# Kernel tuning notes

Measured on AMD Instinct MI355X. Metric: run time of the kernel, lower is better.

## Reference

```python
import jax, jax.numpy as jnp
import numpy as np


def setup_inputs() -> dict:
    key = jax.random.key(0)
    ks = jax.random.split(key, 7)
    T, B, D, H, F = 1024, 128, 256, 256, 128
    inputs = jax.random.normal(ks[0], (T, B, D), dtype=jnp.float32)
    # stacked gate linears (forget, input, update, output): [D+H, 4H]
    Wg = jax.random.normal(ks[1], (D + H, 4 * H), dtype=jnp.float32) / np.sqrt(D + H)
    bg = jax.random.normal(ks[2], (4 * H,), dtype=jnp.float32) * 0.01
    # stacked per-gate FFNs: Linear(H->F), ReLU, Linear(F->H), sigmoid/tanh
    W1 = jax.random.normal(ks[3], (4, H, F), dtype=jnp.float32) / np.sqrt(H)
    b1 = jax.random.normal(ks[4], (4, F), dtype=jnp.float32) * 0.01
    W2 = jax.random.normal(ks[5], (4, F, H), dtype=jnp.float32) / np.sqrt(F)
    b2 = jax.random.normal(ks[6], (4, H), dtype=jnp.float32) * 0.01
    return {"inputs": inputs, "Wg": Wg, "bg": bg, "W1": W1, "b1": b1, "W2": W2, "b2": b2}


def reference(inputs, Wg, bg, W1, b1, W2, b2):
    T, B, D = inputs.shape
    H = W2.shape[-1]

    def step(carry, x):
        hx, cx = carry
        comb = jnp.concatenate([x, hx], axis=1)              # [B, D+H]
        z = (comb @ Wg + bg).reshape(B, 4, H)                # stacked gate linears
        z = jnp.transpose(z, (1, 0, 2))                      # [4, B, H]
        h1 = jax.nn.relu(jnp.einsum('gbh,ghf->gbf', z, W1) + b1[:, None, :])
        z2 = jnp.einsum('gbf,gfh->gbh', h1, W2) + b2[:, None, :]  # [4, B, H]
        f = jax.nn.sigmoid(z2[0])
        i = jax.nn.sigmoid(z2[1])
        g = jnp.tanh(z2[2])
        o = jax.nn.sigmoid(z2[3])
        cx = f * cx + i * g
        hx = o * jnp.tanh(cx)
        return (hx, cx), hx

    h0 = jnp.zeros((B, H), dtype=inputs.dtype)
    c0 = jnp.zeros((B, H), dtype=inputs.dtype)
    (hx, cx), outputs = jax.lax.scan(step, (h0, c0), inputs)
    return outputs, (hx, cx)
```

## Files before the change

### kernel.cpp

```cpp
#include <hip/hip_runtime.h>
#include <hip/hip_fp16.h>
#include <cstdint>

#define T_STEPS 1024
#define BATCH   128
#define DIM     256
#define HID     256
#define FF      128
#define CHUNK   8

typedef _Float16 h2 __attribute__((ext_vector_type(2)));

#define WGXP_OFF 0
#define WGHP_OFF 262144
#define W1P_OFF  524288
#define W2P_OFF  655360
#define WS_HALFS 786432
#define EX_BYTE_OFF 1572864
#define EX_WORDS    262144
#define WS_SPLIT4_BYTES (EX_BYTE_OFF + EX_WORDS * 4)

#define KEEPU4(v) asm volatile("" : "+v"((v).x), "+v"((v).y), "+v"((v).z), "+v"((v).w))

__device__ __forceinline__ float sigmoidf_(float x) {
    return 1.0f / (1.0f + __expf(-x));
}
__device__ __forceinline__ float tanhf_(float x) {
    float e = __expf(2.0f * x);
    return 1.0f - 2.0f / (e + 1.0f);
}
__device__ __forceinline__ float fdot2_(h2 a, h2 b, float c) {
#if __has_builtin(__builtin_amdgcn_fdot2)
    return __builtin_amdgcn_fdot2(a, b, c, false);
#else
    return fmaf((float)a.x, (float)b.x, fmaf((float)a.y, (float)b.y, c));
#endif
}

union U4H { uint4 u; h2 h[4]; };
union HU  { unsigned short u; _Float16 h; };

__global__ __launch_bounds__(256)
void convert_kernel(const float* __restrict__ Wg,
                    const float* __restrict__ W1,
                    const float* __restrict__ W2,
                    _Float16* __restrict__ ws)
{
    int i = blockIdx.x * 256 + threadIdx.x;
    if (i < 524288) {
        int k = i >> 10, c = i & 1023;
        if (k < 256) {
            ws[WGXP_OFF + (((size_t)(k >> 3) << 10) + c) * 8 + (k & 7)] = (_Float16)Wg[i];
        } else {
            int k2 = k - 256;
            ws[WGHP_OFF + (((size_t)(k2 >> 3) << 10) + c) * 8 + (k2 & 7)] = (_Float16)Wg[i];
        }
    } else if (i < 655360) {
        int j = i - 524288;
        int g = j >> 15, k = (j >> 7) & 255, f = j & 127;
        ws[W1P_OFF + (((size_t)((g << 5) + (k >> 3)) << 7) + f) * 8 + (k & 7)] = (_Float16)W1[j];
    } else if (i < 786432) {
        int j = i - 655360;
        int g = j >> 15, f = (j >> 8) & 127, h = j & 255;
        ws[W2P_OFF + (((size_t)((g << 4) + (f >> 3)) << 8) + h) * 8 + (f & 7)] = (_Float16)W2[j];
    }
}

__global__ __launch_bounds__(512)
void exinit_kernel(unsigned* __restrict__ ex) {
    int i = blockIdx.x * 512 + threadIdx.x;
    if (i < EX_WORDS) ex[i] = 0u;
}

__global__ __launch_bounds__(512, 1)
void qlstm_split4L_kernel(const float* __restrict__ x,
                          const _Float16* __restrict__ ws,
                          unsigned* ex,
                          const float* __restrict__ bg,
                          const float* __restrict__ b1,
                          const float* __restrict__ b2,
                          float* __restrict__ out)
{
    const int blk = blockIdx.x;
    const int g   = blk >> 6;
    const int bp  = blk & 63;
    const int tid = threadIdx.x;

    __shared__ __align__(16) uint4   wgh_lds[8192];
    __shared__ __align__(16) _Float16 xc[2 * CHUNK * DIM];
    __shared__ __align__(16) _Float16 zxc[2 * CHUNK * 256];
    __shared__ __align__(16) _Float16 ch2buf[512];
    __shared__ __align__(16) _Float16 zh[512];
    __shared__ __align__(16) _Float16 h1h[256];
    __shared__ float pbuf[1024];

    const uint4* __restrict__ wgxp = reinterpret_cast<const uint4*>(ws + WGXP_OFF);
    const uint4* __restrict__ wghp = reinterpret_cast<const uint4*>(ws + WGHP_OFF);
    const uint4* __restrict__ w1p  = reinterpret_cast<const uint4*>(ws + W1P_OFF);
    const uint4* __restrict__ w2p  = reinterpret_cast<const uint4*>(ws + W2P_OFF);

    const int cc   = tid & 255;
    const int kh16 = (tid >> 8) << 4;
    const int kq8  = ((tid >> 7) & 3) << 3;
    const int ffi  = tid & 127;
    const int fh8  = (tid >> 8) << 3;

    #pragma unroll
    for (int j = 0; j < 16; ++j) {
        int idx = j * 512 + tid;
        int k8 = idx >> 8, c = idx & 255;
        wgh_lds[idx] = wghp[(k8 << 10) + (g << 8) + c];
    }

    const float rbg = bg[(g << 8) + cc];
    const float rb2 = b2[(g << 8) + cc];
    const float rb1 = b1[(g << 7) + ffi];

    uint4 w1_r[8], w2_r[8];
    #pragma unroll
    for (int j = 0; j < 8; ++j)  w1_r[j] = w1p[(((g << 5) + kq8 + j) << 7) + ffi];
    #pragma unroll
    for (int j = 0; j < 8; ++j)  w2_r[j] = w2p[(((g << 4) + fh8 + j) << 8) + cc];
    #pragma unroll
    for (int j = 0; j < 8; ++j)  KEEPU4(w1_r[j]);
    #pragma unroll
    for (int j = 0; j < 8; ++j)  KEEPU4(w2_r[j]);

    ch2buf[tid] = (_Float16)0.0f;
    float c_reg = 0.0f;
    __syncthreads();

    for (int t0 = 0; t0 < T_STEPS; t0 += CHUNK) {
        #pragma unroll
        for (int j = 0; j < 2; ++j) {
            int i4 = j * 512 + tid;
            int bl = i4 >> 9, rem = i4 & 511, tl = rem >> 6, d4 = rem & 63;
            float4 v = reinterpret_cast<const float4*>(
                x + ((size_t)(t0 + tl) * BATCH + bp + (bl << 6)) * DIM)[d4];
            int base = bl * 2048 + tl * 256 + (d4 << 2);
            xc[base + 0] = (_Float16)v.x;
            xc[base + 1] = (_Float16)v.y;
            xc[base + 2] = (_Float16)v.z;
            xc[base + 3] = (_Float16)v.w;
        }
        __syncthreads();

        {
            const int th = tid >> 8;
            const U4H* xcv = reinterpret_cast<const U4H*>(xc);
            float acc[2][4];
            #pragma unroll
            for (int bl = 0; bl < 2; ++bl)
                #pragma unroll
                for (int j = 0; j < 4; ++j) acc[bl][j] = rbg;
            for (int k8 = 0; k8 < 32; ++k8) {
                U4H w; w.u = wgxp[(k8 << 10) + (g << 8) + cc];
                #pragma unroll
                for (int bl = 0; bl < 2; ++bl) {
                    #pragma unroll
                    for (int j = 0; j < 4; ++j) {
                        U4H xv; xv.u = xcv[bl * 256 + (th * 4 + j) * 32 + k8].u;
                        acc[bl][j] = fdot2_(xv.h[0], w.h[0], acc[bl][j]);
                        acc[bl][j] = fdot2_(xv.h[1], w.h[1], acc[bl][j]);
                        acc[bl][j] = fdot2_(xv.h[2], w.h[2], acc[bl][j]);
                        acc[bl][j] = fdot2_(xv.h[3], w.h[3], acc[bl][j]);
                    }
                }
            }
            #pragma unroll
            for (int bl = 0; bl < 2; ++bl)
                #pragma unroll
                for (int j = 0; j < 4; ++j)
                    zxc[bl * 2048 + (th * 4 + j) * 256 + cc] = (_Float16)acc[bl][j];
        }
        __syncthreads();

        for (int tc = 0; tc < CHUNK; ++tc) {
            const int s = t0 + tc;

            {
                const uint4* hA4 = reinterpret_cast<const uint4*>(ch2buf);
                const uint4* hB4 = reinterpret_cast<const uint4*>(ch2buf + 256);
                float aA = 0.0f, aB = 0.0f;
                #pragma unroll
                for (int j = 0; j < 16; ++j) {
                    const int k8 = kh16 + j;
                    U4H w;  w.u  = wgh_lds[k8 * 256 + cc];
                    U4H ha; ha.u = hA4[k8];
                    U4H hb; hb.u = hB4[k8];
                    aA = fdot2_(ha.h[0], w.h[0], aA);
                    aA = fdot2_(ha.h[1], w.h[1], aA);
                    aA = fdot2_(ha.h[2], w.h[2], aA);
                    aA = fdot2_(ha.h[3], w.h[3], aA);
                    aB = fdot2_(hb.h[0], w.h[0], aB);
                    aB = fdot2_(hb.h[1], w.h[1], aB);
                    aB = fdot2_(hb.h[2], w.h[2], aB);
                    aB = fdot2_(hb.h[3], w.h[3], aB);
                }
                pbuf[tid] = aA;
                pbuf[512 + tid] = aB;
            }
            __syncthreads();
            {
                const int bl = tid >> 8, c = tid & 255;
                float z = (float)zxc[bl * 2048 + tc * 256 + c]
                        + pbuf[bl * 512 + c] + pbuf[bl * 512 + 256 + c];
                zh[bl * 256 + c] = (_Float16)z;
            }
            __syncthreads();

            {
                const uint4* zA4 = reinterpret_cast<const uint4*>(zh);
                const uint4* zB4 = reinterpret_cast<const uint4*>(zh + 256);
                float aA = 0.0f, aB = 0.0f;
                #pragma unroll
                for (int j = 0; j < 8; ++j) {
                    const int k8 = kq8 + j;
                    U4H w;  w.u  = w1_r[j];
                    U4H za; za.u = zA4[k8];
                    U4H zb; zb.u = zB4[k8];
                    aA = fdot2_(za.h[0], w.h[0], aA);
                    aA = fdot2_(za.h[1], w.h[1], aA);
                    aA = fdot2_(za.h[2], w.h[2], aA);
                    aA = fdot2_(za.h[3], w.h[3], aA);
                    aB = fdot2_(zb.h[0], w.h[0], aB);
                    aB = fdot2_(zb.h[1], w.h[1], aB);
                    aB = fdot2_(zb.h[2], w.h[2], aB);
                    aB = fdot2_(zb.h[3], w.h[3], aB);
                }
                pbuf[tid] = aA;
                pbuf[512 + tid] = aB;
            }
            __syncthreads();
            if (tid < 256) {
                const int bl = tid >> 7, f = tid & 127;
                float v = b1[(g << 7) + f]
                        + pbuf[bl * 512 + f] + pbuf[bl * 512 + 128 + f]
                        + pbuf[bl * 512 + 256 + f] + pbuf[bl * 512 + 384 + f];
                h1h[bl * 128 + f] = (_Float16)fmaxf(v, 0.0f);
            }
            __syncthreads();

            {
                const uint4* pA4 = reinterpret_cast<const uint4*>(h1h);
                const uint4* pB4 = reinterpret_cast<const uint4*>(h1h + 128);
                float aA = 0.0f, aB = 0.0f;
                #pragma unroll
                for (int j = 0; j < 8; ++j) {
                    const int f8 = fh8 + j;
                    U4H w;  w.u  = w2_r[j];
                    U4H ha; ha.u = pA4[f8];
                    U4H hb; hb.u = pB4[f8];
                    aA = fdot2_(ha.h[0], w.h[0], aA);
                    aA = fdot2_(ha.h[1], w.h[1], aA);
                    aA = fdot2_(ha.h[2], w.h[2], aA);
                    aA = fdot2_(ha.h[3], w.h[3], aA);
                    aB = fdot2_(hb.h[0], w.h[0], aB);
                    aB = fdot2_(hb.h[1], w.h[1], aB);
                    aB = fdot2_(hb.h[2], w.h[2], aB);
                    aB = fdot2_(hb.h[3], w.h[3], aB);
                }
                pbuf[tid] = aA;
                pbuf[512 + tid] = aB;
            }
            __syncthreads();

            {
                const int bl = tid >> 8, c = tid & 255;
                const int b  = bp + (bl << 6);
                float z2 = rb2 * 0.0f + b2[(g << 8) + c]
                         + pbuf[bl * 512 + c] + pbuf[bl * 512 + 256 + c];
                HU hu; hu.h = (_Float16)z2;
                unsigned word = ((unsigned)(s + 1) << 16) | (unsigned)hu.u;
                unsigned widx = (unsigned)(b * 2048 + g * 512 + ((s & 1) << 8) + c);
                __hip_atomic_store(&ex[widx], word, __ATOMIC_RELAXED, __HIP_MEMORY_SCOPE_AGENT);

                const unsigned base = (unsigned)(b * 2048 + ((s & 1) << 8) + c);
                const unsigned want = (unsigned)(s + 1) << 16;
                unsigned w0, w1, w2, w3;
                for (;;) {
                    w0 = __hip_atomic_load(&ex[base],        __ATOMIC_RELAXED, __HIP_MEMORY_SCOPE_AGENT);
                    w1 = __hip_atomic_load(&ex[base + 512],  __ATOMIC_RELAXED, __HIP_MEMORY_SCOPE_AGENT);
                    w2 = __hip_atomic_load(&ex[base + 1024], __ATOMIC_RELAXED, __HIP_MEMORY_SCOPE_AGENT);
                    w3 = __hip_atomic_load(&ex[base + 1536], __ATOMIC_RELAXED, __HIP_MEMORY_SCOPE_AGENT);
                    unsigned m = ((w0 ^ want) | (w1 ^ want) | (w2 ^ want) | (w3 ^ want)) & 0xFFFF0000u;
                    if (m == 0u) break;
                    __builtin_amdgcn_s_sleep(1);
                }
                HU hf, hi, hg, ho;
                hf.u = (unsigned short)(w0 & 0xFFFFu);
                hi.u = (unsigned short)(w1 & 0xFFFFu);
                hg.u = (unsigned short)(w2 & 0xFFFFu);
                ho.u = (unsigned short)(w3 & 0xFFFFu);
                float fg = sigmoidf_((float)hf.h);
                float ig = sigmoidf_((float)hi.h);
                float gg = tanhf_((float)hg.h);
                float og = sigmoidf_((float)ho.h);
                c_reg = fmaf(fg, c_reg, ig * gg);
                float hh = og * tanhf_(c_reg);
                ch2buf[bl * 256 + c] = (_Float16)hh;
                if (g == 0) {
                    out[((size_t)s * BATCH + b) * HID + c] = hh;
                    if (s == T_STEPS - 1) {
                        const size_t TBH = (size_t)T_STEPS * BATCH * HID;
                        out[TBH + (size_t)b * HID + c] = hh;
                        out[TBH + (size_t)BATCH * HID + (size_t)b * HID + c] = c_reg;
                    }
                }
            }
            __syncthreads();
        }
    }
}

__global__ __launch_bounds__(1024)
void qlstm_chunk_kernel(const float* __restrict__ x,
                        const _Float16* __restrict__ ws,
                        const float* __restrict__ bg,
                        const float* __restrict__ b1,
                        const float* __restrict__ b2,
                        float* __restrict__ out)
{
    const int b   = blockIdx.x;
    const int tid = threadIdx.x;

    __shared__ __align__(16) _Float16 xc[CHUNK * DIM];
    __shared__ __align__(16) _Float16 zxc[CHUNK * 1024];
    __shared__ __align__(16) _Float16 zh[1024];
    __shared__ __align__(16) _Float16 h1h[512];
    __shared__ __align__(16) _Float16 ch2buf[HID];
    __shared__ float z2buf[1024];
    __shared__ float cbuf[HID];
    __shared__ float hbuf[HID];

    const float rbg = bg[tid];
    const float rb1 = (tid < 512) ? b1[tid] : 0.0f;
    const float rb2 = b2[tid];

    if (tid < HID) { cbuf[tid] = 0.0f; hbuf[tid] = 0.0f; ch2buf[tid] = (_Float16)0.0f; }

    const uint4* __restrict__ wgxp = reinterpret_cast<const uint4*>(ws + WGXP_OFF);
    const uint4* __restrict__ wghp = reinterpret_cast<const uint4*>(ws + WGHP_OFF);
    const uint4* __restrict__ w1p  = reinterpret_cast<const uint4*>(ws + W1P_OFF);
    const uint4* __restrict__ w2p  = reinterpret_cast<const uint4*>(ws + W2P_OFF);
    const h2* ch2 = reinterpret_cast<const h2*>(ch2buf);
    const U4H* xcv = reinterpret_cast<const U4H*>(xc);

    for (int t0 = 0; t0 < T_STEPS; t0 += CHUNK) {
        for (int idx = tid; idx < CHUNK * DIM; idx += 1024) {
            int tl = idx >> 8, d = idx & 255;
            xc[tl * DIM + d] = (_Float16)x[((size_t)(t0 + tl) * BATCH + b) * DIM + d];
        }
        __syncthreads();

        {
            float acc[CHUNK];
            #pragma unroll
            for (int tc = 0; tc < CHUNK; ++tc) acc[tc] = rbg;
            for (int k8 = 0; k8 < DIM / 8; ++k8) {
                U4H w; w.u = wgxp[(k8 << 10) + tid];
                #pragma unroll
                for (int tc = 0; tc < CHUNK; ++tc) {
                    U4H xv; xv.u = xcv[tc * (DIM / 8) + k8].u;
                    acc[tc] = fdot2_(xv.h[0], w.h[0], acc[tc]);
                    acc[tc] = fdot2_(xv.h[1], w.h[1], acc[tc]);
                    acc[tc] = fdot2_(xv.h[2], w.h[2], acc[tc]);
                    acc[tc] = fdot2_(xv.h[3], w.h[3], acc[tc]);
                }
            }
            #pragma unroll
            for (int tc = 0; tc < CHUNK; ++tc) zxc[tc * 1024 + tid] = (_Float16)acc[tc];
        }
        __syncthreads();

        for (int tc = 0; tc < CHUNK; ++tc) {
            {
                float acc = (float)zxc[tc * 1024 + tid];
                #pragma unroll 8
                for (int k8 = 0; k8 < HID / 8; ++k8) {
                    U4H w; w.u = wghp[(k8 << 10) + tid];
                    acc = fdot2_(ch2[4 * k8 + 0], w.h[0], acc);
                    acc = fdot2_(ch2[4 * k8 + 1], w.h[1], acc);
                    acc = fdot2_(ch2[4 * k8 + 2], w.h[2], acc);
                    acc = fdot2_(ch2[4 * k8 + 3], w.h[3], acc);
                }
                zh[tid] = (_Float16)acc;
            }
            __syncthreads();

            if (tid < 512) {
                const int g = tid >> 7, f = tid & 127;
                const h2* zp = reinterpret_cast<const h2*>(zh + (g << 8));
                float acc = rb1;
                #pragma unroll 8
                for (int k8 = 0; k8 < HID / 8; ++k8) {
                    U4H w; w.u = w1p[(((g << 5) + k8) << 7) + f];
                    acc = fdot2_(zp[4 * k8 + 0], w.h[0], acc);
                    acc = fdot2_(zp[4 * k8 + 1], w.h[1], acc);
                    acc = fdot2_(zp[4 * k8 + 2], w.h[2], acc);
                    acc = fdot2_(zp[4 * k8 + 3], w.h[3], acc);
                }
                h1h[tid] = (_Float16)fmaxf(acc, 0.0f);
            }
            __syncthreads();

            {
                const int g = tid >> 8, hcol = tid & 255;
                const h2* hp = reinterpret_cast<const h2*>(h1h + (g << 7));
                float acc = rb2;
                #pragma unroll 8
                for (int f8 = 0; f8 < FF / 8; ++f8) {
                    U4H w; w.u = w2p[(((g << 4) + f8) << 8) + hcol];
                    acc = fdot2_(hp[4 * f8 + 0], w.h[0], acc);
                    acc = fdot2_(hp[4 * f8 + 1], w.h[1], acc);
                    acc = fdot2_(hp[4 * f8 + 2], w.h[2], acc);
                    acc = fdot2_(hp[4 * f8 + 3], w.h[3], acc);
                }
                z2buf[tid] = acc;
            }
            __syncthreads();

            if (tid < HID) {
                float zf = z2buf[tid];
                float zi = z2buf[HID + tid];
                float zg = z2buf[2 * HID + tid];
                float zo = z2buf[3 * HID + tid];
                float fg = sigmoidf_(zf);
                float ig = sigmoidf_(zi);
                float gg = tanhf_(zg);
                float og = sigmoidf_(zo);
                float ccv = fmaf(fg, cbuf[tid], ig * gg);
                float hh = og * tanhf_(ccv);
                cbuf[tid] = ccv;
                hbuf[tid] = hh;
                ch2buf[tid] = (_Float16)hh;
                out[((size_t)(t0 + tc) * BATCH + b) * HID + tid] = hh;
            }
            __syncthreads();
        }
    }

    if (tid < HID) {
        const size_t TBH = (size_t)T_STEPS * BATCH * HID;
        out[TBH + (size_t)b * HID + tid] = hbuf[tid];
        out[TBH + (size_t)BATCH * HID + (size_t)b * HID + tid] = cbuf[tid];
    }
}

extern "C" void kernel_launch(void* const* d_in, const int* in_sizes, int n_in,
                              void* d_out, int out_size, void* d_ws, size_t ws_size,
                              hipStream_t stream) {
    const float* x  = (const float*)d_in[0];
    const float* Wg = (const float*)d_in[1];
    const float* bg = (const float*)d_in[2];
    const float* W1 = (const float*)d_in[3];
    const float* b1 = (const float*)d_in[4];
    const float* W2 = (const float*)d_in[5];
    const float* b2 = (const float*)d_in[6];
    float* out = (float*)d_out;
    char* wsc = (char*)d_ws;

    if (ws_size >= (size_t)WS_SPLIT4_BYTES) {
        _Float16* ws = (_Float16*)wsc;
        unsigned* ex = (unsigned*)(wsc + EX_BYTE_OFF);
        convert_kernel<<<WS_HALFS / 256, 256, 0, stream>>>(Wg, W1, W2, ws);
        exinit_kernel<<<EX_WORDS / 512, 512, 0, stream>>>(ex);
        qlstm_split4L_kernel<<<256, 512, 0, stream>>>(x, ws, ex, bg, b1, b2, out);
    } else if (ws_size >= (size_t)WS_HALFS * sizeof(_Float16)) {
        _Float16* ws = (_Float16*)wsc;
        convert_kernel<<<WS_HALFS / 256, 256, 0, stream>>>(Wg, W1, W2, ws);
        qlstm_chunk_kernel<<<BATCH, 1024, 0, stream>>>(x, ws, bg, b1, b2, out);
    }
}
```

Baseline: 4.452 ms.

## Double block size to 1024 threads, keep recurrent weights in registers

The persistent split-gate LSTM kernel now runs 1024 threads per block instead of 512. Each thread holds half as many recurrent Wg_h slices in registers instead of reading them from LDS, and the K-split for every matvec widens to four or eight partial sums combined through a larger pbuf. The input-projection chunk grows from 8 to 16 timesteps and the biases are staged in shared memory. The goal is to cut per-step latency on the serial recurrence, at the cost of wider partial-sum reductions, half-idle threads in the reduction and exchange phases, and more register pressure.

```diff
diff --git a/kernel.cpp b/kernel.cpp
--- a/kernel.cpp
+++ b/kernel.cpp
@@ -7,7 +7,7 @@
 #define DIM     256
 #define HID     256
 #define FF      128
-#define CHUNK   8
+#define CHUNK   16
 
 typedef _Float16 h2 __attribute__((ext_vector_type(2)));
 
@@ -72,8 +72,8 @@
     if (i < EX_WORDS) ex[i] = 0u;
 }
 
-__global__ __launch_bounds__(512, 1)
-void qlstm_split4L_kernel(const float* __restrict__ x,
+__global__ __launch_bounds__(1024, 1)
+void qlstm_split4w_kernel(const float* __restrict__ x,
                           const _Float16* __restrict__ ws,
                           unsigned* ex,
                           const float* __restrict__ bg,
@@ -86,58 +86,53 @@
     const int bp  = blk & 63;
     const int tid = threadIdx.x;
 
-    __shared__ __align__(16) uint4   wgh_lds[8192];
     __shared__ __align__(16) _Float16 xc[2 * CHUNK * DIM];
     __shared__ __align__(16) _Float16 zxc[2 * CHUNK * 256];
     __shared__ __align__(16) _Float16 ch2buf[512];
     __shared__ __align__(16) _Float16 zh[512];
     __shared__ __align__(16) _Float16 h1h[256];
-    __shared__ float pbuf[1024];
+    __shared__ float pbuf[2048];
+    __shared__ float b1s[128], b2s[256];
 
     const uint4* __restrict__ wgxp = reinterpret_cast<const uint4*>(ws + WGXP_OFF);
     const uint4* __restrict__ wghp = reinterpret_cast<const uint4*>(ws + WGHP_OFF);
     const uint4* __restrict__ w1p  = reinterpret_cast<const uint4*>(ws + W1P_OFF);
     const uint4* __restrict__ w2p  = reinterpret_cast<const uint4*>(ws + W2P_OFF);
 
-    const int cc   = tid & 255;
-    const int kh16 = (tid >> 8) << 4;
-    const int kq8  = ((tid >> 7) & 3) << 3;
-    const int ffi  = tid & 127;
-    const int fh8  = (tid >> 8) << 3;
-
-    #pragma unroll
-    for (int j = 0; j < 16; ++j) {
-        int idx = j * 512 + tid;
-        int k8 = idx >> 8, c = idx & 255;
-        wgh_lds[idx] = wghp[(k8 << 10) + (g << 8) + c];
-    }
+    const int cc  = tid & 255;
+    const int kq  = tid >> 8;
+    const int ffi = tid & 127;
+    const int kq8 = tid >> 7;
+
+    uint4 wgh_r[8], w1_r[4], w2_r[4];
+    #pragma unroll
+    for (int j = 0; j < 8; ++j) wgh_r[j] = wghp[(((kq << 3) + j) << 10) + (g << 8) + cc];
+    #pragma unroll
+    for (int j = 0; j < 4; ++j) w1_r[j]  = w1p[(((g << 5) + (kq8 << 2) + j) << 7) + ffi];
+    #pragma unroll
+    for (int j = 0; j < 4; ++j) w2_r[j]  = w2p[(((g << 4) + (kq << 2) + j) << 8) + cc];
+    #pragma unroll
+    for (int j = 0; j < 8; ++j) KEEPU4(wgh_r[j]);
+    #pragma unroll
+    for (int j = 0; j < 4; ++j) KEEPU4(w1_r[j]);
+    #pragma unroll
+    for (int j = 0; j < 4; ++j) KEEPU4(w2_r[j]);
 
     const float rbg = bg[(g << 8) + cc];
-    const float rb2 = b2[(g << 8) + cc];
-    const float rb1 = b1[(g << 7) + ffi];
-
-    uint4 w1_r[8], w2_r[8];
-    #pragma unroll
-    for (int j = 0; j < 8; ++j)  w1_r[j] = w1p[(((g << 5) + kq8 + j) << 7) + ffi];
-    #pragma unroll
-    for (int j = 0; j < 8; ++j)  w2_r[j] = w2p[(((g << 4) + fh8 + j) << 8) + cc];
-    #pragma unroll
-    for (int j = 0; j < 8; ++j)  KEEPU4(w1_r[j]);
-    #pragma unroll
-    for (int j = 0; j < 8; ++j)  KEEPU4(w2_r[j]);
-
-    ch2buf[tid] = (_Float16)0.0f;
+    if (tid < 128) b1s[tid] = b1[(g << 7) + tid];
+    else if (tid < 384) b2s[tid - 128] = b2[(g << 8) + (tid - 128)];
+    if (tid < 512) ch2buf[tid] = (_Float16)0.0f;
     float c_reg = 0.0f;
     __syncthreads();
 
     for (int t0 = 0; t0 < T_STEPS; t0 += CHUNK) {
         #pragma unroll
         for (int j = 0; j < 2; ++j) {
-            int i4 = j * 512 + tid;
-            int bl = i4 >> 9, rem = i4 & 511, tl = rem >> 6, d4 = rem & 63;
+            int i4 = j * 1024 + tid;
+            int bl = i4 >> 10, rem = i4 & 1023, tl = rem >> 6, d4 = rem & 63;
             float4 v = reinterpret_cast<const float4*>(
                 x + ((size_t)(t0 + tl) * BATCH + bp + (bl << 6)) * DIM)[d4];
-            int base = bl * 2048 + tl * 256 + (d4 << 2);
+            int base = bl * 4096 + tl * 256 + (d4 << 2);
             xc[base + 0] = (_Float16)v.x;
             xc[base + 1] = (_Float16)v.y;
             xc[base + 2] = (_Float16)v.z;
@@ -146,7 +141,6 @@
         __syncthreads();
 
         {
-            const int th = tid >> 8;
             const U4H* xcv = reinterpret_cast<const U4H*>(xc);
             float acc[2][4];
             #pragma unroll
@@ -159,7 +153,7 @@
                 for (int bl = 0; bl < 2; ++bl) {
                     #pragma unroll
                     for (int j = 0; j < 4; ++j) {
-                        U4H xv; xv.u = xcv[bl * 256 + (th * 4 + j) * 32 + k8].u;
+                        U4H xv; xv.u = xcv[bl * 512 + ((kq << 2) + j) * 32 + k8].u;
                         acc[bl][j] = fdot2_(xv.h[0], w.h[0], acc[bl][j]);
                         acc[bl][j] = fdot2_(xv.h[1], w.h[1], acc[bl][j]);
                         acc[bl][j] = fdot2_(xv.h[2], w.h[2], acc[bl][j]);
@@ -171,7 +165,7 @@
             for (int bl = 0; bl < 2; ++bl)
                 #pragma unroll
                 for (int j = 0; j < 4; ++j)
-                    zxc[bl * 2048 + (th * 4 + j) * 256 + cc] = (_Float16)acc[bl][j];
+                    zxc[bl * 4096 + ((kq << 2) + j) * 256 + cc] = (_Float16)acc[bl][j];
         }
         __syncthreads();
 
@@ -183,9 +177,9 @@
                 const uint4* hB4 = reinterpret_cast<const uint4*>(ch2buf + 256);
                 float aA = 0.0f, aB = 0.0f;
                 #pragma unroll
-                for (int j = 0; j < 16; ++j) {
-                    const int k8 = kh16 + j;
-                    U4H w;  w.u  = wgh_lds[k8 * 256 + cc];
+                for (int j = 0; j < 8; ++j) {
+                    const int k8 = (kq << 3) + j;
+                    U4H w;  w.u  = wgh_r[j];
                     U4H ha; ha.u = hA4[k8];
                     U4H hb; hb.u = hB4[k8];
                     aA = fdot2_(ha.h[0], w.h[0], aA);
@@ -197,14 +191,15 @@
                     aB = fdot2_(hb.h[2], w.h[2], aB);
                     aB = fdot2_(hb.h[3], w.h[3], aB);
                 }
-                pbuf[tid] = aA;
-                pbuf[512 + tid] = aB;
-            }
-            __syncthreads();
-            {
+                pbuf[kq * 512 + cc] = aA;
+                pbuf[kq * 512 + 256 + cc] = aB;
+            }
+            __syncthreads();
+            if (tid < 512) {
                 const int bl = tid >> 8, c = tid & 255;
-                float z = (float)zxc[bl * 2048 + tc * 256 + c]
-                        + pbuf[bl * 512 + c] + pbuf[bl * 512 + 256 + c];
+                float z = (float)zxc[bl * 4096 + tc * 256 + c]
+                        + pbuf[bl * 256 + c]        + pbuf[512 + bl * 256 + c]
+                        + pbuf[1024 + bl * 256 + c] + pbuf[1536 + bl * 256 + c];
                 zh[bl * 256 + c] = (_Float16)z;
             }
             __syncthreads();
@@ -214,8 +209,8 @@
                 const uint4* zB4 = reinterpret_cast<const uint4*>(zh + 256);
                 float aA = 0.0f, aB = 0.0f;
                 #pragma unroll
-                for (int j = 0; j < 8; ++j) {
-                    const int k8 = kq8 + j;
+                for (int j = 0; j < 4; ++j) {
+                    const int k8 = (kq8 << 2) + j;
                     U4H w;  w.u  = w1_r[j];
                     U4H za; za.u = zA4[k8];
                     U4H zb; zb.u = zB4[k8];
@@ -228,15 +223,15 @@
                     aB = fdot2_(zb.h[2], w.h[2], aB);
                     aB = fdot2_(zb.h[3], w.h[3], aB);
                 }
-                pbuf[tid] = aA;
-                pbuf[512 + tid] = aB;
+                pbuf[kq8 * 256 + ffi] = aA;
+                pbuf[kq8 * 256 + 128 + ffi] = aB;
             }
             __syncthreads();
             if (tid < 256) {
                 const int bl = tid >> 7, f = tid & 127;
-                float v = b1[(g << 7) + f]
-                        + pbuf[bl * 512 + f] + pbuf[bl * 512 + 128 + f]
-                        + pbuf[bl * 512 + 256 + f] + pbuf[bl * 512 + 384 + f];
+                float v = b1s[f];
+                #pragma unroll
+                for (int q = 0; q < 8; ++q) v += pbuf[q * 256 + bl * 128 + f];
                 h1h[bl * 128 + f] = (_Float16)fmaxf(v, 0.0f);
             }
             __syncthreads();
@@ -246,8 +241,8 @@
                 const uint4* pB4 = reinterpret_cast<const uint4*>(h1h + 128);
                 float aA = 0.0f, aB = 0.0f;
                 #pragma unroll
-                for (int j = 0; j < 8; ++j) {
-                    const int f8 = fh8 + j;
+                for (int j = 0; j < 4; ++j) {
+                    const int f8 = (kq << 2) + j;
                     U4H w;  w.u  = w2_r[j];
                     U4H ha; ha.u = pA4[f8];
                     U4H hb; hb.u = pB4[f8];
@@ -260,16 +255,17 @@
                     aB = fdot2_(hb.h[2], w.h[2], aB);
                     aB = fdot2_(hb.h[3], w.h[3], aB);
                 }
-                pbuf[tid] = aA;
-                pbuf[512 + tid] = aB;
-            }
-            __syncthreads();
-
-            {
+                pbuf[kq * 512 + cc] = aA;
+                pbuf[kq * 512 + 256 + cc] = aB;
+            }
+            __syncthreads();
+
+            if (tid < 512) {
                 const int bl = tid >> 8, c = tid & 255;
                 const int b  = bp + (bl << 6);
-                float z2 = rb2 * 0.0f + b2[(g << 8) + c]
-                         + pbuf[bl * 512 + c] + pbuf[bl * 512 + 256 + c];
+                float z2 = b2s[c]
+                         + pbuf[bl * 256 + c]        + pbuf[512 + bl * 256 + c]
+                         + pbuf[1024 + bl * 256 + c] + pbuf[1536 + bl * 256 + c];
                 HU hu; hu.h = (_Float16)z2;
                 unsigned word = ((unsigned)(s + 1) << 16) | (unsigned)hu.u;
                 unsigned widx = (unsigned)(b * 2048 + g * 512 + ((s & 1) << 8) + c);
@@ -465,7 +461,7 @@
         unsigned* ex = (unsigned*)(wsc + EX_BYTE_OFF);
         convert_kernel<<<WS_HALFS / 256, 256, 0, stream>>>(Wg, W1, W2, ws);
         exinit_kernel<<<EX_WORDS / 512, 512, 0, stream>>>(ex);
-        qlstm_split4L_kernel<<<256, 512, 0, stream>>>(x, ws, ex, bg, b1, b2, out);
+        qlstm_split4w_kernel<<<256, 1024, 0, stream>>>(x, ws, ex, bg, b1, b2, out);
     } else if (ws_size >= (size_t)WS_HALFS * sizeof(_Float16)) {
         _Float16* ws = (_Float16*)wsc;
         convert_kernel<<<WS_HALFS / 256, 256, 0, stream>>>(Wg, W1, W2, ws);
```

Result: slower. 5.209 ms (+17.0%).
